# Optimization experiments

Hardware: AMD Instinct MI355X
Metric: run time of the kernel (lower is better)

The kernel has to match this reference:

```python
import jax, jax.numpy as jnp
import numpy as np

B, S, D = 4, 2048, 1024
H = 4 * D          # expert hidden dim
E_SPEC = 4         # num specific experts
E_SHR = 2          # num shared experts
TOP_K = 2


def setup_inputs() -> dict:
    key = jax.random.key(0)
    ks = jax.random.split(key, 16)
    s = 0.02
    return {
        "x": jax.random.normal(ks[0], (B, S, D), jnp.float32),
        # specific experts (stacked over expert axis)
        "spec_w1": jax.random.normal(ks[1], (E_SPEC, D, H), jnp.float32) * s,
        "spec_b1": jnp.zeros((E_SPEC, H), jnp.float32),
        "spec_w2": jax.random.normal(ks[2], (E_SPEC, H, D), jnp.float32) * s,
        "spec_b2": jnp.zeros((E_SPEC, D), jnp.float32),
        "spec_rw": jax.random.normal(ks[3], (D, E_SPEC), jnp.float32) * s,
        "spec_rb": jnp.zeros((E_SPEC,), jnp.float32),
        # shared experts
        "shr_w1": jax.random.normal(ks[4], (E_SHR, D, H), jnp.float32) * s,
        "shr_b1": jnp.zeros((E_SHR, H), jnp.float32),
        "shr_w2": jax.random.normal(ks[5], (E_SHR, H, D), jnp.float32) * s,
        "shr_b2": jnp.zeros((E_SHR, D), jnp.float32),
        "shr_rw": jax.random.normal(ks[6], (D, E_SHR), jnp.float32) * s,
        "shr_rb": jnp.zeros((E_SHR,), jnp.float32),
    }


def _expert_mlp(xf, w1, b1, w2, b2):
    # xf: [T, D]; w1: [E, D, H]; w2: [E, H, D] -> [E, T, D]
    h = jax.nn.gelu(jnp.einsum("td,edh->eth", xf, w1) + b1[:, None, :],
                    approximate=False)
    return jnp.einsum("eth,ehd->etd", h, w2) + b2[:, None, :]


def reference(x, spec_w1, spec_b1, spec_w2, spec_b2, spec_rw, spec_rb,
              shr_w1, shr_b1, shr_w2, shr_b2, shr_rw, shr_rb):
    b, s, d = x.shape
    xf = x.reshape(-1, d)                      # [T, D]
    T = xf.shape[0]

    # --- specific (top-k) routing ---
    spec_probs = jax.nn.softmax(xf @ spec_rw + spec_rb, axis=-1)   # [T, E]
    topk_probs, topk_idx = jax.lax.top_k(spec_probs, TOP_K)        # [T, K]

    # aux load-balancing loss
    counts = jnp.zeros((E_SPEC,), jnp.float32).at[topk_idx.reshape(-1)].add(1.0)
    fraction = counts / (T * TOP_K)
    aux_loss = E_SPEC * jnp.sum(fraction * spec_probs.mean(axis=0))

    # gate[t, e] = sum_k topk_probs[t,k] * 1[topk_idx[t,k]==e]
    gate = jnp.sum(jax.nn.one_hot(topk_idx, E_SPEC, dtype=xf.dtype)
                   * topk_probs[..., None], axis=1)                # [T, E]

    spec_out_e = _expert_mlp(xf, spec_w1, spec_b1, spec_w2, spec_b2)  # [E, T, D]
    specific_out = jnp.einsum("te,etd->td", gate, spec_out_e)

    # --- shared (dense) experts ---
    shr_probs = jax.nn.softmax(xf @ shr_rw + shr_rb, axis=-1)      # [T, E_shr]
    shr_out_e = _expert_mlp(xf, shr_w1, shr_b1, shr_w2, shr_b2)    # [E_shr, T, D]
    shared_out = jnp.einsum("te,etd->td", shr_probs, shr_out_e)

    final = (specific_out + shared_out).reshape(b, s, d)
    return final, aux_loss
```

## Files before the change

kernel.cpp:

```cpp
#include <hip/hip_runtime.h>
#include <hip/hip_bf16.h>

#define T_TOK 8192
#define DDIM 1024
#define HDIM 4096

typedef __bf16 bf16;
typedef bf16 bf16x8 __attribute__((ext_vector_type(8)));
typedef float f32x4 __attribute__((ext_vector_type(4)));

#define ASM_VMCNT(n) asm volatile("s_waitcnt vmcnt(" #n ")" ::: "memory")
#define MFMA16(a, b, c) __builtin_amdgcn_mfma_f32_16x16x32_bf16((a), (b), (c), 0, 0, 0)
#define G8_BAR __builtin_amdgcn_s_barrier()
#define G8_WAIT                                            \
  asm volatile("s_waitcnt lgkmcnt(0)" ::: "memory");       \
  __builtin_amdgcn_sched_barrier(0)

__device__ __forceinline__ void gl_lds16(const void* g, void* l) {
  __builtin_amdgcn_global_load_lds(
      (const __attribute__((address_space(1))) unsigned int*)g,
      (__attribute__((address_space(3))) unsigned int*)l, 16, 0, 0);
}

__device__ __forceinline__ float gelu_f(float v) {
// ... 53 lines not shown
    const float l0 = p0 + srb[0], l1 = p1 + srb[1];
    const float l2 = p2 + srb[2], l3 = p3 + srb[3];
    const float m = fmaxf(fmaxf(l0, l1), fmaxf(l2, l3));
    const float e0 = expf(l0 - m), e1 = expf(l1 - m);
    const float e2 = expf(l2 - m), e3 = expf(l3 - m);
    const float s = e0 + e1 + e2 + e3;
    float pr[4] = {e0 / s, e1 / s, e2 / s, e3 / s};
    int i1 = 0; float v1 = pr[0];
#pragma unroll
    for (int e = 1; e < 4; ++e) if (pr[e] > v1) { v1 = pr[e]; i1 = e; }
    int i2 = -1; float v2 = -1.0f;
#pragma unroll
    for (int e = 0; e < 4; ++e)
      if (e != i1 && pr[e] > v2) { v2 = pr[e]; i2 = e; }
    float g[4] = {0, 0, 0, 0};
    g[i1] = v1; g[i2] = v2;
    float* gr = gate + (size_t)t * 8;
    gr[0] = g[0]; gr[1] = g[1]; gr[2] = g[2]; gr[3] = g[3];
    const float h0 = p4 + hrb[0], h1 = p5 + hrb[1];
    const float mh = fmaxf(h0, h1);
    const float q0 = expf(h0 - mh), q1 = expf(h1 - mh);
    const float qs = q0 + q1;
    gr[4] = q0 / qs; gr[5] = q1 / qs; gr[6] = 0; gr[7] = 0;
    probs4[t] = make_float4(pr[0], pr[1], pr[2], pr[3]);
    top2[t] = i1 | (i2 << 8);
  }
}

__global__ __launch_bounds__(256) void transpose_convert6(
    const float* __restrict__ spec_w, const float* __restrict__ shr_w,
    bf16* __restrict__ dst, int R, int C) {
  __shared__ float tile[32][33];
  const int z = blockIdx.z;
  const float* src = (z < 4) ? spec_w + (size_t)z * R * C
                             : shr_w + (size_t)(z - 4) * R * C;
  bf16* d = dst + (size_t)z * R * C;
  const int c0 = blockIdx.x * 32, r0 = blockIdx.y * 32;
  const int tx = threadIdx.x & 31, ty = threadIdx.x >> 5;
#pragma unroll
  for (int i = 0; i < 4; ++i)
    tile[ty + 8 * i][tx] = src[(size_t)(r0 + ty + 8 * i) * C + c0 + tx];
  __syncthreads();
#pragma unroll
  for (int i = 0; i < 4; ++i)
    d[(size_t)(c0 + ty + 8 * i) * R + r0 + tx] = (bf16)tile[tx][ty + 8 * i];
}

__global__ __launch_bounds__(1024) void scan_build(
    const int* __restrict__ top2, const float4* __restrict__ probs4,
    int* __restrict__ meta, int* __restrict__ lists, int2* __restrict__ tpos,
    float* __restrict__ auxg) {
  __shared__ unsigned long long sc[1024];
  __shared__ float4 rp[512];
  const int tid = threadIdx.x;

  int ee[8];
  unsigned long long c = 0;
  float4 ps = make_float4(0.f, 0.f, 0.f, 0.f);
#pragma unroll
  for (int j = 0; j < 8; ++j) {
    const int t = tid * 8 + j;
    const int p = top2[t];
    ee[j] = p;
    const int a = p & 15, b = (p >> 8) & 15;
    c += (1ULL << (16 * a)) + (1ULL << (16 * b));
    const float4 pv = probs4[t];
    ps.x += pv.x; ps.y += pv.y; ps.z += pv.z; ps.w += pv.w;
  }
  sc[tid] = c;
  __syncthreads();
  for (int off = 1; off < 1024; off <<= 1) {
    const unsigned long long mine = sc[tid];
    const unsigned long long prev = (tid >= off) ? sc[tid - off] : 0ULL;
    __syncthreads();
    sc[tid] = mine + prev;
    __syncthreads();
  }
  const unsigned long long incl = sc[tid];
  const unsigned long long tot = sc[1023];
  const unsigned long long excl = incl - c;
  int q0 = (int)(excl & 0xffff), q1 = (int)((excl >> 16) & 0xffff);
  int q2 = (int)((excl >> 32) & 0xffff), q3 = (int)((excl >> 48) & 0xffff);
#pragma unroll
  for (int j = 0; j < 8; ++j) {
    const int t = tid * 8 + j;
    const int a = ee[j] & 15, b = (ee[j] >> 8) & 15;
    const int pa = (a == 0) ? q0 : (a == 1) ? q1 : (a == 2) ? q2 : q3;
    lists[a * 8192 + pa] = t;
    q0 += (a == 0); q1 += (a == 1); q2 += (a == 2); q3 += (a == 3);
    const int pb = (b == 0) ? q0 : (b == 1) ? q1 : (b == 2) ? q2 : q3;
    lists[b * 8192 + pb] = t;
    q0 += (b == 0); q1 += (b == 1); q2 += (b == 2); q3 += (b == 3);
    tpos[t] = make_int2(a * 8192 + pa, b * 8192 + pb);
  }
  if (tid == 1023) {
    const int c0 = (int)(tot & 0xffff), c1 = (int)((tot >> 16) & 0xffff);
    const int c2 = (int)((tot >> 32) & 0xffff), c3 = (int)((tot >> 48) & 0xffff);
    meta[24] = c0; meta[25] = c1; meta[26] = c2; meta[27] = c3;
    auxg[0] = (float)c0; auxg[1] = (float)c1;
    auxg[2] = (float)c2; auxg[3] = (float)c3;
    const int nb0 = (c0 + 255) >> 8, nb1 = (c1 + 255) >> 8;
    const int nb2 = (c2 + 255) >> 8, nb3 = (c3 + 255) >> 8;
    const int ch0 = (nb0 + 3) >> 2, ch1 = (nb1 + 3) >> 2;
    const int ch2 = (nb2 + 3) >> 2, ch3 = (nb3 + 3) >> 2;
    meta[34] = 0;
    meta[35] = nb0 * 256;
    meta[36] = meta[35] + nb1 * 256;
    meta[37] = meta[36] + nb2 * 256;
    meta[40] = 0;
    meta[41] = 64 * ch0;
    meta[42] = meta[41] + 64 * ch1;
    meta[43] = meta[42] + 64 * ch2;
    meta[44] = meta[43] + 64 * ch3;
    meta[46] = 0;
    meta[47] = 32 * ch0;
    meta[48] = meta[47] + 32 * ch1;
    meta[49] = meta[48] + 32 * ch2;
    meta[50] = meta[49] + 32 * ch3;
  }
  if (tid >= 512) rp[tid - 512] = ps;
  __syncthreads();
  if (tid < 512) {
    const float4 o = rp[tid];
    ps.x += o.x; ps.y += o.y; ps.z += o.z; ps.w += o.w;
  }
  for (int w = 256; w >= 1; w >>= 1) {
    __syncthreads();
    if (tid >= w && tid < 2 * w) rp[tid - w] = ps;
    __syncthreads();
    if (tid < w) {
      const float4 o = rp[tid];
      ps.x += o.x; ps.y += o.y; ps.z += o.z; ps.w += o.w;
    }
  }
  if (tid == 0) {
    auxg[4] = ps.x; auxg[5] = ps.y; auxg[6] = ps.z; auxg[7] = ps.w;
  }
}

__global__ void aux_finalize(const float* __restrict__ auxg,
                             float* __restrict__ outp) {
  float a = 0.0f;
#pragma unroll
  for (int e = 0; e < 4; ++e)
    a += (auxg[e] / (float)(T_TOK * 2)) * (auxg[4 + e] / (float)T_TOK);
  outp[0] = 4.0f * a;
}

template <int KIND>
__global__ __launch_bounds__(512, 2) void g8(
    const bf16* __restrict__ A, const bf16* __restrict__ Bw,
    const float* __restrict__ bias, bf16* __restrict__ h_all, int N,
    int CH_M, int CH_N, const int* __restrict__ meta,
    const int* __restrict__ lists, const float* __restrict__ gate) {
  __shared__ __align__(1024) bf16 Alds[2 * 256 * 64];
  __shared__ __align__(1024) bf16 Blds[2 * 256 * 64];

  const int tid = threadIdx.x;
  const int lane = tid & 63, wid = tid >> 6;
  const int wm = wid >> 2, wn = wid & 3;
  const int lr = lane & 15, lg = lane >> 4;

  int bm, bn, hb = 0, s = 0;
  const bf16* Bp = Bw;
  const float* biasp = bias;
  if constexpr (KIND == 0) {
    const int xcd = blockIdx.x & 7, idx = blockIdx.x >> 3;
    bm = (xcd >> 1) * CH_M + idx / CH_N;
    bn = (xcd & 1) * CH_N + idx % CH_N;
  } else {
    const int b = blockIdx.x;
    if (b >= meta[44]) return;
    s = (b >= meta[41]) + (b >= meta[42]) + (b >= meta[43]);
    const int local = b - meta[40 + s];
    const int nbm = (meta[24 + s] + 255) >> 8;
    const int CHm = (nbm + 3) >> 2;
    if (local >= 64 * CHm) return;
    const int xc = local & 7, idx = local >> 3;
    bm = (xc >> 1) * CHm + idx / 8;
    bn = (xc & 1) * 8 + idx % 8;
    if (bm >= nbm) return;
    hb = meta[34 + s];
    Bp = Bw + (size_t)s * DDIM * HDIM;
    biasp = bias + (size_t)s * HDIM;
  }
  const int K = DDIM;
  const int NT = K >> 6;

  const int rl = tid >> 3;
  const int cbs = ((tid * 16) & 127) ^ ((rl & 7) << 4);
  int ar[4];
#pragma unroll
  for (int c = 0; c < 4; ++c) ar[c] = bm * 256 + c * 64 + rl;
  if constexpr (KIND != 0) {
    const int* lp = lists + s * 8192;
#pragma unroll
    for (int c = 0; c < 4; ++c) {
      const int t = lp[ar[c]];
      ar[c] = t < 0 ? 0 : t;
    }
  }
  const bf16* sA[4];
  const bf16* sB[4];
#pragma unroll
  for (int c = 0; c < 4; ++c) {
    sA[c] = A + (size_t)ar[c] * K + (cbs >> 1);
    sB[c] = Bp + (size_t)(bn * 256 + c * 64 + rl) * K + (cbs >> 1);
  }
  char* const ldsA = (char*)Alds;
  char* const ldsB = (char*)Blds;
  const int wb = wid * 1024;

  const int ax0 = (lg * 16) ^ ((lr & 7) << 4);
  const int ax1 = ax0 ^ 64;
  const int aro = (wm * 128 + lr) * 128;
  const int bro = (wn * 64 + lr) * 128;
  const char* const A0 = (const char*)Alds + aro + ax0;
  const char* const A1 = (const char*)Alds + aro + ax1;
  const char* const B0 = (const char*)Blds + bro + ax0;
  const char* const B1 = (const char*)Blds + bro + ax1;

  f32x4 acc[8][4] = {};
  bf16x8 af[4][2], b01[2][2], b23[2][2];

#define G8_RA(BOFF, MB)                                               \
  _Pragma("unroll") for (int i = 0; i < 4; ++i) {                     \
    af[i][0] = *(const bf16x8*)(A0 + (BOFF) + ((MB) + i) * 2048);     \
    af[i][1] = *(const bf16x8*)(A1 + (BOFF) + ((MB) + i) * 2048);     \
  }
#define G8_RB(BOFF, DST, NB)                                          \
  _Pragma("unroll") for (int i = 0; i < 2; ++i) {                     \
    DST[i][0] = *(const bf16x8*)(B0 + (BOFF) + ((NB) + i) * 2048);    \
    DST[i][1] = *(const bf16x8*)(B1 + (BOFF) + ((NB) + i) * 2048);    \
  }
#define G8_MMA(MB, NB, BSRC)                                          \
  __builtin_amdgcn_s_setprio(1);                                      \
  _Pragma("unroll") for (int i = 0; i < 4; ++i)                       \
    _Pragma("unroll") for (int j = 0; j < 2; ++j) {                   \
      acc[(MB) + i][(NB) + j] =                                       \
          MFMA16(af[i][0], BSRC[j][0], acc[(MB) + i][(NB) + j]);      \
      acc[(MB) + i][(NB) + j] =                                       \
          MFMA16(af[i][1], BSRC[j][1], acc[(MB) + i][(NB) + j]);      \
    }                                                                 \
  __builtin_amdgcn_s_setprio(0);
#define G8_STG_B(T, C, BUFO)                                          \
  gl_lds16(sB[C] + (size_t)(T) * 64, ldsB + (BUFO) + (C) * 8192 + wb);
#define G8_STG_A(T, C, BUFO)                                          \
  gl_lds16(sA[C] + (size_t)(T) * 64, ldsA + (BUFO) + (C) * 8192 + wb);

  G8_STG_B(0, 0, 0) G8_STG_B(0, 1, 0) G8_STG_B(0, 2, 0) G8_STG_B(0, 3, 0)
  G8_STG_A(0, 0, 0) G8_STG_A(0, 1, 0) G8_STG_A(0, 2, 0) G8_STG_A(0, 3, 0)
  G8_STG_B(1, 0, 32768) G8_STG_B(1, 1, 32768)
  G8_STG_B(1, 2, 32768) G8_STG_B(1, 3, 32768)
  G8_STG_A(1, 0, 32768) G8_STG_A(1, 1, 32768)
  G8_STG_A(1, 2, 32768) G8_STG_A(1, 3, 32768)
  ASM_VMCNT(8);
  G8_BAR;

  for (int t = 0; t < NT; t += 2) {
    const bool stg = (t + 2) < NT;
    G8_RA(0, 0);
    G8_RB(0, b01, 0);
    G8_BAR; G8_WAIT;
    G8_MMA(0, 0, b01);
    G8_BAR;
    G8_RB(0, b23, 2);
    G8_BAR; G8_WAIT;
    G8_MMA(0, 2, b23);
    G8_BAR;
    G8_RA(0, 4);
    if (stg) { G8_STG_B(t + 2, 0, 0) G8_STG_B(t + 2, 1, 0) }
    G8_BAR; G8_WAIT;
    G8_MMA(4, 0, b01);
    G8_BAR;
    if (stg) { G8_STG_B(t + 2, 2, 0) G8_STG_B(t + 2, 3, 0) }
    G8_MMA(4, 2, b23);
    if (stg) ASM_VMCNT(4); else ASM_VMCNT(0);
    G8_BAR;
    G8_RA(32768, 0);
    G8_RB(32768, b01, 0);
    if (stg) { G8_STG_A(t + 2, 0, 0) G8_STG_A(t + 2, 1, 0) }
    G8_BAR; G8_WAIT;
    G8_MMA(0, 0, b01);
    G8_BAR;
    G8_RB(32768, b23, 2);
    if (stg) { G8_STG_A(t + 2, 2, 0) G8_STG_A(t + 2, 3, 0) }
    G8_BAR; G8_WAIT;
    G8_MMA(0, 2, b23);
    G8_BAR;
    G8_RA(32768, 4);
    if (stg) {
      G8_STG_B(t + 3, 0, 32768) G8_STG_B(t + 3, 1, 32768)
      G8_STG_B(t + 3, 2, 32768) G8_STG_B(t + 3, 3, 32768)
    }
    G8_BAR; G8_WAIT;
    G8_MMA(4, 0, b01);
    G8_BAR;
    if (stg) {
      G8_STG_A(t + 3, 0, 32768) G8_STG_A(t + 3, 1, 32768)
      G8_STG_A(t + 3, 2, 32768) G8_STG_A(t + 3, 3, 32768)
    }
    G8_MMA(4, 2, b23);
    if (stg) ASM_VMCNT(8);
    G8_BAR;
  }

  const int colb = bn * 256 + wn * 64;
  const int rowb = bm * 256 + wm * 128 + lg * 4;
  float bv[4];
#pragma unroll
  for (int nf = 0; nf < 4; ++nf) bv[nf] = biasp[colb + nf * 16 + lr];
  const int sgid = (KIND == 0) ? 4 + (bn >> 4) : s;
#pragma unroll
  for (int mf = 0; mf < 8; ++mf) {
    float gv[4];
#pragma unroll
    for (int r = 0; r < 4; ++r) {
      const int lrow = rowb + mf * 16 + r;
      if constexpr (KIND == 0) {
        gv[r] = gate[(size_t)lrow * 8 + sgid];
      } else {
        const int tok = lists[s * 8192 + lrow];
        gv[r] = tok >= 0 ? gate[(size_t)tok * 8 + sgid] : 0.0f;
      }
    }
#pragma unroll
    for (int nf = 0; nf < 4; ++nf) {
      const int col = colb + nf * 16 + lr;
#pragma unroll
      for (int r = 0; r < 4; ++r) {
        const int row = hb + rowb + mf * 16 + r;
        h_all[(size_t)row * N + col] =
            (bf16)(gv[r] * gelu_f(acc[mf][nf][r] + bv[nf]));
      }
    }
  }
}

__global__ __launch_bounds__(512, 2) void g2sh(
    const bf16* __restrict__ A, const bf16* __restrict__ w2_0,
    const bf16* __restrict__ w2_1, const float* __restrict__ b2,
    float* __restrict__ out, const float* __restrict__ gate) {
  __shared__ __align__(1024) bf16 Alds[2 * 256 * 64];
  __shared__ __align__(1024) bf16 Blds[2 * 128 * 64];

  const int tid = threadIdx.x;
  const int lane = tid & 63, wid = tid >> 6;
  const int wm = wid >> 2, wn = wid & 3;
  const int lr = lane & 15, lg = lane >> 4;

  const int xcd = blockIdx.x & 7, idx = blockIdx.x >> 3;
  const int bm = (xcd >> 1) * 8 + idx / 4;
  const int bn = (xcd & 1) * 4 + idx % 4;
  const int lda = 8192, N = DDIM;
  const int NT = 128;

  const int L = tid * 16;
  const int rl = L >> 7;
  const int colb = (L & 127) ^ ((rl & 7) << 4);

  const int ar0 = bm * 256 + rl;
  const bf16* sAc0 = A + (size_t)ar0 * lda + (colb >> 1);
  const bf16* sAc1 = A + (size_t)(ar0 + 64) * lda + (colb >> 1);
  const bf16* sAc2 = A + (size_t)(ar0 + 128) * lda + (colb >> 1);
  const bf16* sAc3 = A + (size_t)(ar0 + 192) * lda + (colb >> 1);
  const bf16* pB[2][2];
  pB[0][0] = w2_0 + (size_t)(bn * 128 + rl) * 4096 + (colb >> 1);
  pB[0][1] = w2_0 + (size_t)(bn * 128 + 64 + rl) * 4096 + (colb >> 1);
  pB[1][0] = w2_1 + (size_t)(bn * 128 + rl) * 4096 + (colb >> 1);
  pB[1][1] = w2_1 + (size_t)(bn * 128 + 64 + rl) * 4096 + (colb >> 1);

  char* const ldsA = (char*)Alds;
  char* const ldsB = (char*)Blds;
  const int wb = wid * 1024;
  char* const stA[2] = {ldsA + wb, ldsA + 32768 + wb};
  char* const stB[2] = {ldsB + wb, ldsB + 16384 + wb};

  const int ax0 = (lg * 16) ^ ((lr & 7) << 4);
  const int ax1 = ax0 ^ 64;
  const int aro = (wm * 128 + lr) * 128;
  const int bro = (wn * 32 + lr) * 128;
  const char* const Ak0[2] = {ldsA + aro + ax0, ldsA + 32768 + aro + ax0};
  const char* const Ak1[2] = {ldsA + aro + ax1, ldsA + 32768 + aro + ax1};
  const char* const Bk0[2] = {ldsB + bro + ax0, ldsB + 16384 + bro + ax0};
  const char* const Bk1[2] = {ldsB + bro + ax1, ldsB + 16384 + bro + ax1};

  f32x4 acc[8][2] = {};

#define G2S_STB(T, DST)                                                   \
  {                                                                       \
    const int hh = (T) >> 6;                                              \
    const size_t oo = (size_t)((T) & 63) * 64;                            \
    gl_lds16(pB[hh][0] + oo, DST);                                        \
    gl_lds16(pB[hh][1] + oo, DST + 8192);                                 \
  }

  gl_lds16(sAc0, stA[0]);
  gl_lds16(sAc1, stA[0] + 8192);
  gl_lds16(sAc2, stA[0] + 16384);
  gl_lds16(sAc3, stA[0] + 24576);
  G2S_STB(0, stB[0])
  G2S_STB(1, stB[1])
  gl_lds16(sAc0 + 64, stA[1]);
  gl_lds16(sAc1 + 64, stA[1] + 8192);
  ASM_VMCNT(4);
  __builtin_amdgcn_s_barrier();

  for (int kt0 = 0; kt0 < NT; kt0 += 2) {
#pragma unroll
    for (int par = 0; par < 2; ++par) {
      const int kt = kt0 + par;
      const int cur = par, oth = par ^ 1;
      const bool st1 = (kt + 1) < NT, st2 = (kt + 2) < NT;
      const size_t ko1 = (size_t)(kt + 1) << 6, ko2 = (size_t)(kt + 2) << 6;
      const char* Ac0 = Ak0[cur]; const char* Ac1 = Ak1[cur];
      const char* Bc0 = Bk0[cur]; const char* Bc1 = Bk1[cur];

      bf16x8 af[4][2], bfr[2][2];

#pragma unroll
      for (int mf = 0; mf < 4; ++mf) {
        af[mf][0] = *(const bf16x8*)(Ac0 + mf * 2048);
        af[mf][1] = *(const bf16x8*)(Ac1 + mf * 2048);
      }
      bfr[0][0] = *(const bf16x8*)(Bc0);
      bfr[0][1] = *(const bf16x8*)(Bc1);
      if (st1) {
        gl_lds16(sAc2 + ko1, stA[oth] + 16384);
        gl_lds16(sAc3 + ko1, stA[oth] + 24576);
      }
      __builtin_amdgcn_s_barrier();
      asm volatile("s_waitcnt lgkmcnt(0)" ::: "memory");
      __builtin_amdgcn_sched_barrier(0);
      __builtin_amdgcn_s_setprio(1);
#pragma unroll
      for (int mf = 0; mf < 4; ++mf) {
        acc[mf][0] = MFMA16(af[mf][0], bfr[0][0], acc[mf][0]);
        acc[mf][0] = MFMA16(af[mf][1], bfr[0][1], acc[mf][0]);
      }
      __builtin_amdgcn_s_setprio(0);
      __builtin_amdgcn_s_barrier();

      bfr[1][0] = *(const bf16x8*)(Bc0 + 2048);
      bfr[1][1] = *(const bf16x8*)(Bc1 + 2048);
      __builtin_amdgcn_s_barrier();
      asm volatile("s_waitcnt lgkmcnt(0)" ::: "memory");
      __builtin_amdgcn_sched_barrier(0);
      __builtin_amdgcn_s_setprio(1);
#pragma unroll
      for (int mf = 0; mf < 4; ++mf) {
        acc[mf][1] = MFMA16(af[mf][0], bfr[1][0], acc[mf][1]);
        acc[mf][1] = MFMA16(af[mf][1], bfr[1][1], acc[mf][1]);
      }
      __builtin_amdgcn_s_setprio(0);
      __builtin_amdgcn_s_barrier();

#pragma unroll
      for (int mf = 0; mf < 4; ++mf) {
        af[mf][0] = *(const bf16x8*)(Ac0 + 8192 + mf * 2048);
        af[mf][1] = *(const bf16x8*)(Ac1 + 8192 + mf * 2048);
      }
      if (st2) G2S_STB(kt + 2, stB[cur])
      __builtin_amdgcn_s_barrier();
      asm volatile("s_waitcnt lgkmcnt(0)" ::: "memory");
      __builtin_amdgcn_sched_barrier(0);
      __builtin_amdgcn_s_setprio(1);
#pragma unroll
      for (int mf = 0; mf < 4; ++mf) {
        acc[4 + mf][0] = MFMA16(af[mf][0], bfr[0][0], acc[4 + mf][0]);
        acc[4 + mf][0] = MFMA16(af[mf][1], bfr[0][1], acc[4 + mf][0]);
      }
      __builtin_amdgcn_s_setprio(0);
      __builtin_amdgcn_s_barrier();

      if (st2) {
        gl_lds16(sAc0 + ko2, stA[cur]);
        gl_lds16(sAc1 + ko2, stA[cur] + 8192);
      }
      __builtin_amdgcn_s_setprio(1);
#pragma unroll
      for (int mf = 0; mf < 4; ++mf) {
        acc[4 + mf][1] = MFMA16(af[mf][0], bfr[1][0], acc[4 + mf][1]);
        acc[4 + mf][1] = MFMA16(af[mf][1], bfr[1][1], acc[4 + mf][1]);
      }
      __builtin_amdgcn_s_setprio(0);
      if (st2) {
        ASM_VMCNT(4);
        __builtin_amdgcn_s_barrier();
      } else if (st1) {
        ASM_VMCNT(0);
        __builtin_amdgcn_s_barrier();
      }
    }
  }

  const int colb2 = bn * 128 + wn * 32;
  const int rowb = bm * 256 + wm * 128 + lg * 4;
  float bv0[2], bv1[2];
#pragma unroll
  for (int nf = 0; nf < 2; ++nf) {
    bv0[nf] = b2[colb2 + nf * 16 + lr];
    bv1[nf] = b2[1024 + colb2 + nf * 16 + lr];
  }
#pragma unroll
  for (int mf = 0; mf < 8; ++mf) {
    float g4[4], g5[4];
#pragma unroll
    for (int r = 0; r < 4; ++r) {
      const size_t row = rowb + mf * 16 + r;
      g4[r] = gate[row * 8 + 4];
      g5[r] = gate[row * 8 + 5];
    }
#pragma unroll
    for (int nf = 0; nf < 2; ++nf) {
      const int col = colb2 + nf * 16 + lr;
#pragma unroll
      for (int r = 0; r < 4; ++r) {
        out[(size_t)(rowb + mf * 16 + r) * N + col] =
            acc[mf][nf][r] + g4[r] * bv0[nf] + g5[r] * bv1[nf];
      }
    }
  }
}

template <int PMODE>
__global__ __launch_bounds__(512, 2) void g2sp(
    const bf16* __restrict__ h_all, const bf16* __restrict__ w2t,
    const float* __restrict__ spec_b2, float* __restrict__ out,
    bf16* __restrict__ P, const float* __restrict__ gate,
    const int* __restrict__ meta, const int* __restrict__ lists, int e) {
  __shared__ __align__(1024) bf16 Alds[2 * 256 * 64];
  __shared__ __align__(1024) bf16 Blds[2 * 128 * 64];

  const int tid = threadIdx.x;
  const int lane = tid & 63, wid = tid >> 6;
  const int wm = wid >> 2, wn = wid & 3;
  const int lr = lane & 15, lg = lane >> 4;

  int bm, bn, s = e;
  if constexpr (PMODE == 1) {
    const int b = blockIdx.x;
    if (b >= meta[50]) return;
    s = (b >= meta[47]) + (b >= meta[48]) + (b >= meta[49]);
    const int local = b - meta[46 + s];
    const int nbm = (meta[24 + s] + 255) >> 8;
    const int CHm = (nbm + 3) >> 2;
    if (local >= 32 * CHm) return;
    const int xc = local & 7, idx = local >> 3;
    bm = (xc >> 1) * CHm + idx / 4;
    bn = (xc & 1) * 4 + idx % 4;
    if (bm >= nbm) return;
  } else {
    const int nbm = (meta[24 + e] + 255) >> 8;
    const int CHm = (nbm + 3) >> 2;
    if (blockIdx.x >= 8 * CHm * 4) return;
    const int xc = blockIdx.x & 7, idx = blockIdx.x >> 3;
    bm = (xc >> 1) * CHm + idx / 4;
    bn = (xc & 1) * 4 + idx % 4;
    if (bm >= nbm) return;
  }
  const int hb = meta[34 + s];
  const bf16* B = w2t + (size_t)s * DDIM * HDIM;
  const float* bias = spec_b2 + (size_t)s * DDIM;
  const int K = HDIM, N = DDIM;
  const int NT = K >> 6;

  const int L = tid * 16;
  const int rl = L >> 7;
  const int colb = (L & 127) ^ ((rl & 7) << 4);

  const int ar0 = hb + bm * 256 + rl;
  const bf16* sAc0 = h_all + (size_t)ar0 * K + (colb >> 1);
  const bf16* sAc1 = h_all + (size_t)(ar0 + 64) * K + (colb >> 1);
  const bf16* sAc2 = h_all + (size_t)(ar0 + 128) * K + (colb >> 1);
  const bf16* sAc3 = h_all + (size_t)(ar0 + 192) * K + (colb >> 1);
  const bf16* sB = B + (size_t)(bn * 128 + rl) * K + (colb >> 1);

  char* const ldsA = (char*)Alds;
  char* const ldsB = (char*)Blds;
  const int wb = wid * 1024;
  char* const stA[2] = {ldsA + wb, ldsA + 32768 + wb};
  char* const stB[2] = {ldsB + wb, ldsB + 16384 + wb};

  const int ax0 = (lg * 16) ^ ((lr & 7) << 4);
  const int ax1 = ax0 ^ 64;
  const int aro = (wm * 128 + lr) * 128;
  const int bro = (wn * 32 + lr) * 128;
  const char* const Ak0[2] = {ldsA + aro + ax0, ldsA + 32768 + aro + ax0};
  const char* const Ak1[2] = {ldsA + aro + ax1, ldsA + 32768 + aro + ax1};
  const char* const Bk0[2] = {ldsB + bro + ax0, ldsB + 16384 + bro + ax0};
  const char* const Bk1[2] = {ldsB + bro + ax1, ldsB + 16384 + bro + ax1};

  f32x4 acc[8][2] = {};

  gl_lds16(sAc0, stA[0]);
  gl_lds16(sAc1, stA[0] + 8192);
  gl_lds16(sAc2, stA[0] + 16384);
  gl_lds16(sAc3, stA[0] + 24576);
  gl_lds16(sB, stB[0]);
  gl_lds16(sB + (size_t)64 * K, stB[0] + 8192);
  gl_lds16(sB + 64, stB[1]);
  gl_lds16(sB + (size_t)64 * K + 64, stB[1] + 8192);
  gl_lds16(sAc0 + 64, stA[1]);
  gl_lds16(sAc1 + 64, stA[1] + 8192);
  ASM_VMCNT(4);
  __builtin_amdgcn_s_barrier();

  for (int kt0 = 0; kt0 < NT; kt0 += 2) {
#pragma unroll
    for (int par = 0; par < 2; ++par) {
      const int kt = kt0 + par;
      const int cur = par, oth = par ^ 1;
      const bool st1 = (kt + 1) < NT, st2 = (kt + 2) < NT;
      const size_t ko1 = (size_t)(kt + 1) << 6, ko2 = (size_t)(kt + 2) << 6;
      const char* Ac0 = Ak0[cur]; const char* Ac1 = Ak1[cur];
      const char* Bc0 = Bk0[cur]; const char* Bc1 = Bk1[cur];

      bf16x8 af[4][2], bfr[2][2];

#pragma unroll
      for (int mf = 0; mf < 4; ++mf) {
        af[mf][0] = *(const bf16x8*)(Ac0 + mf * 2048);
        af[mf][1] = *(const bf16x8*)(Ac1 + mf * 2048);
      }
      bfr[0][0] = *(const bf16x8*)(Bc0);
      bfr[0][1] = *(const bf16x8*)(Bc1);
      if (st1) {
        gl_lds16(sAc2 + ko1, stA[oth] + 16384);
        gl_lds16(sAc3 + ko1, stA[oth] + 24576);
      }
      __builtin_amdgcn_s_barrier();
      asm volatile("s_waitcnt lgkmcnt(0)" ::: "memory");
      __builtin_amdgcn_sched_barrier(0);
      __builtin_amdgcn_s_setprio(1);
#pragma unroll
      for (int mf = 0; mf < 4; ++mf) {
        acc[mf][0] = MFMA16(af[mf][0], bfr[0][0], acc[mf][0]);
        acc[mf][0] = MFMA16(af[mf][1], bfr[0][1], acc[mf][0]);
      }
      __builtin_amdgcn_s_setprio(0);
      __builtin_amdgcn_s_barrier();

      bfr[1][0] = *(const bf16x8*)(Bc0 + 2048);
      bfr[1][1] = *(const bf16x8*)(Bc1 + 2048);
      __builtin_amdgcn_s_barrier();
      asm volatile("s_waitcnt lgkmcnt(0)" ::: "memory");
      __builtin_amdgcn_sched_barrier(0);
      __builtin_amdgcn_s_setprio(1);
#pragma unroll
      for (int mf = 0; mf < 4; ++mf) {
        acc[mf][1] = MFMA16(af[mf][0], bfr[1][0], acc[mf][1]);
        acc[mf][1] = MFMA16(af[mf][1], bfr[1][1], acc[mf][1]);
      }
      __builtin_amdgcn_s_setprio(0);
      __builtin_amdgcn_s_barrier();

#pragma unroll
      for (int mf = 0; mf < 4; ++mf) {
        af[mf][0] = *(const bf16x8*)(Ac0 + 8192 + mf * 2048);
        af[mf][1] = *(const bf16x8*)(Ac1 + 8192 + mf * 2048);
      }
      if (st2) {
        gl_lds16(sB + ko2, stB[cur]);
        gl_lds16(sB + (size_t)64 * K + ko2, stB[cur] + 8192);
      }
      __builtin_amdgcn_s_barrier();
      asm volatile("s_waitcnt lgkmcnt(0)" ::: "memory");
      __builtin_amdgcn_sched_barrier(0);
      __builtin_amdgcn_s_setprio(1);
#pragma unroll
      for (int mf = 0; mf < 4; ++mf) {
        acc[4 + mf][0] = MFMA16(af[mf][0], bfr[0][0], acc[4 + mf][0]);
        acc[4 + mf][0] = MFMA16(af[mf][1], bfr[0][1], acc[4 + mf][0]);
      }
      __builtin_amdgcn_s_setprio(0);
      __builtin_amdgcn_s_barrier();

      if (st2) {
        gl_lds16(sAc0 + ko2, stA[cur]);
        gl_lds16(sAc1 + ko2, stA[cur] + 8192);
      }
      __builtin_amdgcn_s_setprio(1);
#pragma unroll
      for (int mf = 0; mf < 4; ++mf) {
        acc[4 + mf][1] = MFMA16(af[mf][0], bfr[1][0], acc[4 + mf][1]);
        acc[4 + mf][1] = MFMA16(af[mf][1], bfr[1][1], acc[4 + mf][1]);
      }
      __builtin_amdgcn_s_setprio(0);
      if (st2) {
        ASM_VMCNT(4);
        __builtin_amdgcn_s_barrier();
      } else if (st1) {
        ASM_VMCNT(0);
        __builtin_amdgcn_s_barrier();
      }
    }
  }

  const int colb2 = bn * 128 + wn * 32;
  const int rowb = bm * 256 + wm * 128 + lg * 4;
  float bv[2];
#pragma unroll
  for (int nf = 0; nf < 2; ++nf) bv[nf] = bias[colb2 + nf * 16 + lr];
  const int* lp = lists + s * 8192;
#pragma unroll
  for (int mf = 0; mf < 8; ++mf) {
    int tok[4]; float gv[4];
#pragma unroll
    for (int r = 0; r < 4; ++r) {
      tok[r] = lp[rowb + mf * 16 + r];
      gv[r] = tok[r] >= 0 ? gate[(size_t)tok[r] * 8 + s] : 0.0f;
    }
#pragma unroll
    for (int nf = 0; nf < 2; ++nf) {
      const int col = colb2 + nf * 16 + lr;
#pragma unroll
      for (int r = 0; r < 4; ++r) {
        const float v = acc[mf][nf][r] + gv[r] * bv[nf];
        if constexpr (PMODE == 1) {
          P[(size_t)(hb + rowb + mf * 16 + r) * N + col] = (bf16)v;
        } else {
          if (tok[r] >= 0) out[(size_t)tok[r] * N + col] += v;
        }
      }
    }
  }
}

__global__ __launch_bounds__(256) void reduce_spec(
    const bf16* __restrict__ P, const int2* __restrict__ tpos,
    const int* __restrict__ meta, float* __restrict__ out) {
  const int t = blockIdx.x;
  const int c = threadIdx.x * 4;
  const int2 tp = tpos[t];
  const int ea = tp.x >> 13, pa = tp.x & 8191;
  const int eb = tp.y >> 13, pb = tp.y & 8191;
  const size_t ra = (size_t)(meta[34 + ea] + pa) * DDIM + c;
  const size_t rb = (size_t)(meta[34 + eb] + pb) * DDIM + c;
  const bf16x8* pav = (const bf16x8*)&P[ra];
  float4 o = *(float4*)&out[(size_t)t * DDIM + c];
  const bf16* A4 = &P[ra];
  const bf16* B4 = &P[rb];
  o.x += (float)A4[0] + (float)B4[0];
  o.y += (float)A4[1] + (float)B4[1];
  o.z += (float)A4[2] + (float)B4[2];
  o.w += (float)A4[3] + (float)B4[3];
  (void)pav;
  *(float4*)&out[(size_t)t * DDIM + c] = o;
}

extern "C" void kernel_launch(void* const* d_in, const int* in_sizes, int n_in,
                              void* d_out, int out_size, void* d_ws,
                              size_t ws_size, hipStream_t stream) {
  const float* x = (const float*)d_in[0];
  const float* spec_w1 = (const float*)d_in[1];
  const float* spec_b1 = (const float*)d_in[2];
  const float* spec_w2 = (const float*)d_in[3];
  const float* spec_b2 = (const float*)d_in[4];
  const float* spec_rw = (const float*)d_in[5];
  const float* spec_rb = (const float*)d_in[6];
  const float* shr_w1 = (const float*)d_in[7];
  const float* shr_b1 = (const float*)d_in[8];
  const float* shr_w2 = (const float*)d_in[9];
  const float* shr_b2 = (const float*)d_in[10];
  const float* shr_rw = (const float*)d_in[11];
  const float* shr_rb = (const float*)d_in[12];
  float* out = (float*)d_out;

  char* ws = (char*)d_ws;
  const size_t DH = (size_t)DDIM * HDIM;
  const size_t OFF_W1 = 16777216;
  const size_t OFF_W2 = OFF_W1 + 50331648;
  const size_t OFF_GATE = OFF_W2 + 50331648;
  const size_t OFF_AUX = OFF_GATE + 262144;
  const size_t OFF_META = OFF_AUX + 256;
  const size_t OFF_LIST = OFF_META + 256;
  const size_t OFF_T2 = OFF_LIST + 131072;
  const size_t OFF_P4 = OFF_T2 + 32768;
  const size_t OFF_TPOS = OFF_P4 + 131072 + 1024;
  const size_t OFF_H = OFF_TPOS + 65536;
  const size_t H_BYTES = (size_t)17408 * HDIM * 2;
  const size_t OFF_P = OFF_H + H_BYTES;
  const size_t P_BYTES = (size_t)17408 * DDIM * 2;
  bf16* xb = (bf16*)ws;
  bf16* w1t = (bf16*)(ws + OFF_W1);
  bf16* w2t = (bf16*)(ws + OFF_W2);
  float* gate = (float*)(ws + OFF_GATE);
  float* auxg = (float*)(ws + OFF_AUX);
  int* meta = (int*)(ws + OFF_META);
  int* lists = (int*)(ws + OFF_LIST);
  int* top2 = (int*)(ws + OFF_T2);
  float4* probs4 = (float4*)(ws + OFF_P4);
  int2* tpos = (int2*)(ws + OFF_TPOS);
  bf16* h = (bf16*)(ws + OFF_H);
  bf16* P = (bf16*)(ws + OFF_P);

  const bool ppath = ws_size >= OFF_P + P_BYTES;

  hipMemsetAsync(lists, 0xFF, 4 * 8192 * 4, stream);

  conv_router<<<T_TOK / 4, 256, 0, stream>>>(x, xb, spec_rw, spec_rb, shr_rw,
                                             shr_rb, gate, probs4, top2);
  scan_build<<<1, 1024, 0, stream>>>(top2, probs4, meta, lists, tpos, auxg);

  transpose_convert6<<<dim3(HDIM / 32, DDIM / 32, 6), 256, 0, stream>>>(
      spec_w1, shr_w1, w1t, DDIM, HDIM);
  transpose_convert6<<<dim3(DDIM / 32, HDIM / 32, 6), 256, 0, stream>>>(
      spec_w2, shr_w2, w2t, HDIM, DDIM);

  g8<0><<<1024, 512, 0, stream>>>(xb, w1t + 4 * DH, shr_b1, h, 8192,
                                  8, 16, meta, lists, gate);
  g2sh<<<256, 512, 0, stream>>>(h, w2t + 4 * DH, w2t + 5 * DH, shr_b2, out,
                                gate);
  g8<1><<<2048, 512, 0, stream>>>(xb, w1t, spec_b1, h, 4096,
                                  0, 8, meta, lists, gate);
  if (ppath) {
    g2sp<1><<<1024, 512, 0, stream>>>(h, w2t, spec_b2, out, P, gate, meta,
                                      lists, 0);
    reduce_spec<<<T_TOK, 256, 0, stream>>>(P, tpos, meta, out);
  } else {
    for (int e = 0; e < 4; ++e)
      g2sp<0><<<256, 512, 0, stream>>>(h, w2t, spec_b2, out, nullptr, gate,
                                       meta, lists, e);
  }
  aux_finalize<<<1, 1, 0, stream>>>(auxg, out + (size_t)T_TOK * DDIM);
}
```

Baseline: 1.062 ms.

## Move gate scaling to second GEMM epilogue and split shared expert down-projection

The gate multiply moves out of the first GEMM's GELU epilogue, so h stores plain GELU activations, and is applied in the second GEMM epilogue as gate*(acc+bias). The fused two-expert shared down-projection kernel is replaced by a generic g2k kernel launched twice, the second accumulating into out with a read-modify-write. The partial-sum buffer P now reuses the w1t workspace region, so the P path always runs and the per-expert fallback is removed. This trims the first GEMM epilogue and drops the workspace-size dependence, at the cost of an extra launch and an extra read and write of out for the shared experts.

```diff
diff --git a/kernel.cpp b/kernel.cpp
--- a/kernel.cpp
+++ b/kernel.cpp
@@ -229,7 +229,7 @@
     const bf16* __restrict__ A, const bf16* __restrict__ Bw,
     const float* __restrict__ bias, bf16* __restrict__ h_all, int N,
     int CH_M, int CH_N, const int* __restrict__ meta,
-    const int* __restrict__ lists, const float* __restrict__ gate) {
+    const int* __restrict__ lists) {
   __shared__ __align__(1024) bf16 Alds[2 * 256 * 64];
   __shared__ __align__(1024) bf16 Blds[2 * 256 * 64];
 
@@ -383,41 +383,28 @@
   }
 
   const int colb = bn * 256 + wn * 64;
-  const int rowb = bm * 256 + wm * 128 + lg * 4;
+  const int rowb = hb + bm * 256 + wm * 128 + lg * 4;
   float bv[4];
 #pragma unroll
   for (int nf = 0; nf < 4; ++nf) bv[nf] = biasp[colb + nf * 16 + lr];
-  const int sgid = (KIND == 0) ? 4 + (bn >> 4) : s;
-#pragma unroll
-  for (int mf = 0; mf < 8; ++mf) {
-    float gv[4];
-#pragma unroll
-    for (int r = 0; r < 4; ++r) {
-      const int lrow = rowb + mf * 16 + r;
-      if constexpr (KIND == 0) {
-        gv[r] = gate[(size_t)lrow * 8 + sgid];
-      } else {
-        const int tok = lists[s * 8192 + lrow];
-        gv[r] = tok >= 0 ? gate[(size_t)tok * 8 + sgid] : 0.0f;
-      }
-    }
+#pragma unroll
+  for (int mf = 0; mf < 8; ++mf)
 #pragma unroll
     for (int nf = 0; nf < 4; ++nf) {
       const int col = colb + nf * 16 + lr;
 #pragma unroll
       for (int r = 0; r < 4; ++r) {
-        const int row = hb + rowb + mf * 16 + r;
-        h_all[(size_t)row * N + col] =
-            (bf16)(gv[r] * gelu_f(acc[mf][nf][r] + bv[nf]));
-      }
-    }
-  }
-}
-
-__global__ __launch_bounds__(512, 2) void g2sh(
-    const bf16* __restrict__ A, const bf16* __restrict__ w2_0,
-    const bf16* __restrict__ w2_1, const float* __restrict__ b2,
-    float* __restrict__ out, const float* __restrict__ gate) {
+        const int row = rowb + mf * 16 + r;
+        h_all[(size_t)row * N + col] = (bf16)gelu_f(acc[mf][nf][r] + bv[nf]);
+      }
+    }
+}
+
+template <int EMODE>
+__global__ __launch_bounds__(512, 2) void g2k(
+    const bf16* __restrict__ A, int lda, const bf16* __restrict__ B,
+    const float* __restrict__ bias, float* __restrict__ out,
+    const float* __restrict__ gate, int gidx) {
   __shared__ __align__(1024) bf16 Alds[2 * 256 * 64];
   __shared__ __align__(1024) bf16 Blds[2 * 128 * 64];
 
@@ -429,8 +416,8 @@
   const int xcd = blockIdx.x & 7, idx = blockIdx.x >> 3;
   const int bm = (xcd >> 1) * 8 + idx / 4;
   const int bn = (xcd & 1) * 4 + idx % 4;
-  const int lda = 8192, N = DDIM;
-  const int NT = 128;
+  const int K = HDIM, N = DDIM;
+  const int NT = K >> 6;
 
   const int L = tid * 16;
   const int rl = L >> 7;
@@ -441,216 +428,6 @@
   const bf16* sAc1 = A + (size_t)(ar0 + 64) * lda + (colb >> 1);
   const bf16* sAc2 = A + (size_t)(ar0 + 128) * lda + (colb >> 1);
   const bf16* sAc3 = A + (size_t)(ar0 + 192) * lda + (colb >> 1);
-  const bf16* pB[2][2];
-  pB[0][0] = w2_0 + (size_t)(bn * 128 + rl) * 4096 + (colb >> 1);
-  pB[0][1] = w2_0 + (size_t)(bn * 128 + 64 + rl) * 4096 + (colb >> 1);
-  pB[1][0] = w2_1 + (size_t)(bn * 128 + rl) * 4096 + (colb >> 1);
-  pB[1][1] = w2_1 + (size_t)(bn * 128 + 64 + rl) * 4096 + (colb >> 1);
-
-  char* const ldsA = (char*)Alds;
-  char* const ldsB = (char*)Blds;
-  const int wb = wid * 1024;
-  char* const stA[2] = {ldsA + wb, ldsA + 32768 + wb};
-  char* const stB[2] = {ldsB + wb, ldsB + 16384 + wb};
-
-  const int ax0 = (lg * 16) ^ ((lr & 7) << 4);
-  const int ax1 = ax0 ^ 64;
-  const int aro = (wm * 128 + lr) * 128;
-  const int bro = (wn * 32 + lr) * 128;
-  const char* const Ak0[2] = {ldsA + aro + ax0, ldsA + 32768 + aro + ax0};
-  const char* const Ak1[2] = {ldsA + aro + ax1, ldsA + 32768 + aro + ax1};
-  const char* const Bk0[2] = {ldsB + bro + ax0, ldsB + 16384 + bro + ax0};
-  const char* const Bk1[2] = {ldsB + bro + ax1, ldsB + 16384 + bro + ax1};
-
-  f32x4 acc[8][2] = {};
-
-#define G2S_STB(T, DST)                                                   \
-  {                                                                       \
-    const int hh = (T) >> 6;                                              \
-    const size_t oo = (size_t)((T) & 63) * 64;                            \
-    gl_lds16(pB[hh][0] + oo, DST);                                        \
-    gl_lds16(pB[hh][1] + oo, DST + 8192);                                 \
-  }
-
-  gl_lds16(sAc0, stA[0]);
-  gl_lds16(sAc1, stA[0] + 8192);
-  gl_lds16(sAc2, stA[0] + 16384);
-  gl_lds16(sAc3, stA[0] + 24576);
-  G2S_STB(0, stB[0])
-  G2S_STB(1, stB[1])
-  gl_lds16(sAc0 + 64, stA[1]);
-  gl_lds16(sAc1 + 64, stA[1] + 8192);
-  ASM_VMCNT(4);
-  __builtin_amdgcn_s_barrier();
-
-  for (int kt0 = 0; kt0 < NT; kt0 += 2) {
-#pragma unroll
-    for (int par = 0; par < 2; ++par) {
-      const int kt = kt0 + par;
-      const int cur = par, oth = par ^ 1;
-      const bool st1 = (kt + 1) < NT, st2 = (kt + 2) < NT;
-      const size_t ko1 = (size_t)(kt + 1) << 6, ko2 = (size_t)(kt + 2) << 6;
-      const char* Ac0 = Ak0[cur]; const char* Ac1 = Ak1[cur];
-      const char* Bc0 = Bk0[cur]; const char* Bc1 = Bk1[cur];
-
-      bf16x8 af[4][2], bfr[2][2];
-
-#pragma unroll
-      for (int mf = 0; mf < 4; ++mf) {
-        af[mf][0] = *(const bf16x8*)(Ac0 + mf * 2048);
-        af[mf][1] = *(const bf16x8*)(Ac1 + mf * 2048);
-      }
-      bfr[0][0] = *(const bf16x8*)(Bc0);
-      bfr[0][1] = *(const bf16x8*)(Bc1);
-      if (st1) {
-        gl_lds16(sAc2 + ko1, stA[oth] + 16384);
-        gl_lds16(sAc3 + ko1, stA[oth] + 24576);
-      }
-      __builtin_amdgcn_s_barrier();
-      asm volatile("s_waitcnt lgkmcnt(0)" ::: "memory");
-      __builtin_amdgcn_sched_barrier(0);
-      __builtin_amdgcn_s_setprio(1);
-#pragma unroll
-      for (int mf = 0; mf < 4; ++mf) {
-        acc[mf][0] = MFMA16(af[mf][0], bfr[0][0], acc[mf][0]);
-        acc[mf][0] = MFMA16(af[mf][1], bfr[0][1], acc[mf][0]);
-      }
-      __builtin_amdgcn_s_setprio(0);
-      __builtin_amdgcn_s_barrier();
-
-      bfr[1][0] = *(const bf16x8*)(Bc0 + 2048);
-      bfr[1][1] = *(const bf16x8*)(Bc1 + 2048);
-      __builtin_amdgcn_s_barrier();
-      asm volatile("s_waitcnt lgkmcnt(0)" ::: "memory");
-      __builtin_amdgcn_sched_barrier(0);
-      __builtin_amdgcn_s_setprio(1);
-#pragma unroll
-      for (int mf = 0; mf < 4; ++mf) {
-        acc[mf][1] = MFMA16(af[mf][0], bfr[1][0], acc[mf][1]);
-        acc[mf][1] = MFMA16(af[mf][1], bfr[1][1], acc[mf][1]);
-      }
-      __builtin_amdgcn_s_setprio(0);
-      __builtin_amdgcn_s_barrier();
-
-#pragma unroll
-      for (int mf = 0; mf < 4; ++mf) {
-        af[mf][0] = *(const bf16x8*)(Ac0 + 8192 + mf * 2048);
-        af[mf][1] = *(const bf16x8*)(Ac1 + 8192 + mf * 2048);
-      }
-      if (st2) G2S_STB(kt + 2, stB[cur])
-      __builtin_amdgcn_s_barrier();
-      asm volatile("s_waitcnt lgkmcnt(0)" ::: "memory");
-      __builtin_amdgcn_sched_barrier(0);
-      __builtin_amdgcn_s_setprio(1);
-#pragma unroll
-      for (int mf = 0; mf < 4; ++mf) {
-        acc[4 + mf][0] = MFMA16(af[mf][0], bfr[0][0], acc[4 + mf][0]);
-        acc[4 + mf][0] = MFMA16(af[mf][1], bfr[0][1], acc[4 + mf][0]);
-      }
-      __builtin_amdgcn_s_setprio(0);
-      __builtin_amdgcn_s_barrier();
-
-      if (st2) {
-        gl_lds16(sAc0 + ko2, stA[cur]);
-        gl_lds16(sAc1 + ko2, stA[cur] + 8192);
-      }
-      __builtin_amdgcn_s_setprio(1);
-#pragma unroll
-      for (int mf = 0; mf < 4; ++mf) {
-        acc[4 + mf][1] = MFMA16(af[mf][0], bfr[1][0], acc[4 + mf][1]);
-        acc[4 + mf][1] = MFMA16(af[mf][1], bfr[1][1], acc[4 + mf][1]);
-      }
-      __builtin_amdgcn_s_setprio(0);
-      if (st2) {
-        ASM_VMCNT(4);
-        __builtin_amdgcn_s_barrier();
-      } else if (st1) {
-        ASM_VMCNT(0);
-        __builtin_amdgcn_s_barrier();
-      }
-    }
-  }
-
-  const int colb2 = bn * 128 + wn * 32;
-  const int rowb = bm * 256 + wm * 128 + lg * 4;
-  float bv0[2], bv1[2];
-#pragma unroll
-  for (int nf = 0; nf < 2; ++nf) {
-    bv0[nf] = b2[colb2 + nf * 16 + lr];
-    bv1[nf] = b2[1024 + colb2 + nf * 16 + lr];
-  }
-#pragma unroll
-  for (int mf = 0; mf < 8; ++mf) {
-    float g4[4], g5[4];
-#pragma unroll
-    for (int r = 0; r < 4; ++r) {
-      const size_t row = rowb + mf * 16 + r;
-      g4[r] = gate[row * 8 + 4];
-      g5[r] = gate[row * 8 + 5];
-    }
-#pragma unroll
-    for (int nf = 0; nf < 2; ++nf) {
-      const int col = colb2 + nf * 16 + lr;
-#pragma unroll
-      for (int r = 0; r < 4; ++r) {
-        out[(size_t)(rowb + mf * 16 + r) * N + col] =
-            acc[mf][nf][r] + g4[r] * bv0[nf] + g5[r] * bv1[nf];
-      }
-    }
-  }
-}
-
-template <int PMODE>
-__global__ __launch_bounds__(512, 2) void g2sp(
-    const bf16* __restrict__ h_all, const bf16* __restrict__ w2t,
-    const float* __restrict__ spec_b2, float* __restrict__ out,
-    bf16* __restrict__ P, const float* __restrict__ gate,
-    const int* __restrict__ meta, const int* __restrict__ lists, int e) {
-  __shared__ __align__(1024) bf16 Alds[2 * 256 * 64];
-  __shared__ __align__(1024) bf16 Blds[2 * 128 * 64];
-
-  const int tid = threadIdx.x;
-  const int lane = tid & 63, wid = tid >> 6;
-  const int wm = wid >> 2, wn = wid & 3;
-  const int lr = lane & 15, lg = lane >> 4;
-
-  int bm, bn, s = e;
-  if constexpr (PMODE == 1) {
-    const int b = blockIdx.x;
-    if (b >= meta[50]) return;
-    s = (b >= meta[47]) + (b >= meta[48]) + (b >= meta[49]);
-    const int local = b - meta[46 + s];
-    const int nbm = (meta[24 + s] + 255) >> 8;
-    const int CHm = (nbm + 3) >> 2;
-    if (local >= 32 * CHm) return;
-    const int xc = local & 7, idx = local >> 3;
-    bm = (xc >> 1) * CHm + idx / 4;
-    bn = (xc & 1) * 4 + idx % 4;
-    if (bm >= nbm) return;
-  } else {
-    const int nbm = (meta[24 + e] + 255) >> 8;
-    const int CHm = (nbm + 3) >> 2;
-    if (blockIdx.x >= 8 * CHm * 4) return;
-    const int xc = blockIdx.x & 7, idx = blockIdx.x >> 3;
-    bm = (xc >> 1) * CHm + idx / 4;
-    bn = (xc & 1) * 4 + idx % 4;
-    if (bm >= nbm) return;
-  }
-  const int hb = meta[34 + s];
-  const bf16* B = w2t + (size_t)s * DDIM * HDIM;
-  const float* bias = spec_b2 + (size_t)s * DDIM;
-  const int K = HDIM, N = DDIM;
-  const int NT = K >> 6;
-
-  const int L = tid * 16;
-  const int rl = L >> 7;
-  const int colb = (L & 127) ^ ((rl & 7) << 4);
-
-  const int ar0 = hb + bm * 256 + rl;
-  const bf16* sAc0 = h_all + (size_t)ar0 * K + (colb >> 1);
-  const bf16* sAc1 = h_all + (size_t)(ar0 + 64) * K + (colb >> 1);
-  const bf16* sAc2 = h_all + (size_t)(ar0 + 128) * K + (colb >> 1);
-  const bf16* sAc3 = h_all + (size_t)(ar0 + 192) * K + (colb >> 1);
   const bf16* sB = B + (size_t)(bn * 128 + rl) * K + (colb >> 1);
 
   char* const ldsA = (char*)Alds;
@@ -779,6 +556,196 @@
   float bv[2];
 #pragma unroll
   for (int nf = 0; nf < 2; ++nf) bv[nf] = bias[colb2 + nf * 16 + lr];
+#pragma unroll
+  for (int mf = 0; mf < 8; ++mf) {
+    float gv[4];
+#pragma unroll
+    for (int r = 0; r < 4; ++r)
+      gv[r] = gate[(size_t)(rowb + mf * 16 + r) * 8 + gidx];
+#pragma unroll
+    for (int nf = 0; nf < 2; ++nf) {
+      const int col = colb2 + nf * 16 + lr;
+#pragma unroll
+      for (int r = 0; r < 4; ++r) {
+        const float v = acc[mf][nf][r] + bv[nf];
+        const size_t oi = (size_t)(rowb + mf * 16 + r) * N + col;
+        if constexpr (EMODE == 1)
+          out[oi] += gv[r] * v;
+        else
+          out[oi] = gv[r] * v;
+      }
+    }
+  }
+}
+
+__global__ __launch_bounds__(512, 2) void g2sp(
+    const bf16* __restrict__ h_all, const bf16* __restrict__ w2t,
+    const float* __restrict__ spec_b2, bf16* __restrict__ P,
+    const float* __restrict__ gate, const int* __restrict__ meta,
+    const int* __restrict__ lists) {
+  __shared__ __align__(1024) bf16 Alds[2 * 256 * 64];
+  __shared__ __align__(1024) bf16 Blds[2 * 128 * 64];
+
+  const int tid = threadIdx.x;
+  const int lane = tid & 63, wid = tid >> 6;
+  const int wm = wid >> 2, wn = wid & 3;
+  const int lr = lane & 15, lg = lane >> 4;
+
+  const int b = blockIdx.x;
+  if (b >= meta[50]) return;
+  const int s = (b >= meta[47]) + (b >= meta[48]) + (b >= meta[49]);
+  const int local = b - meta[46 + s];
+  const int nbm = (meta[24 + s] + 255) >> 8;
+  const int CHm = (nbm + 3) >> 2;
+  if (local >= 32 * CHm) return;
+  const int xc = local & 7, idx = local >> 3;
+  int bm = (xc >> 1) * CHm + idx / 4;
+  int bn = (xc & 1) * 4 + idx % 4;
+  if (bm >= nbm) return;
+
+  const int hb = meta[34 + s];
+  const bf16* B = w2t + (size_t)s * DDIM * HDIM;
+  const float* bias = spec_b2 + (size_t)s * DDIM;
+  const int K = HDIM, N = DDIM;
+  const int NT = K >> 6;
+
+  const int L = tid * 16;
+  const int rl = L >> 7;
+  const int colb = (L & 127) ^ ((rl & 7) << 4);
+
+  const int ar0 = hb + bm * 256 + rl;
+  const bf16* sAc0 = h_all + (size_t)ar0 * K + (colb >> 1);
+  const bf16* sAc1 = h_all + (size_t)(ar0 + 64) * K + (colb >> 1);
+  const bf16* sAc2 = h_all + (size_t)(ar0 + 128) * K + (colb >> 1);
+  const bf16* sAc3 = h_all + (size_t)(ar0 + 192) * K + (colb >> 1);
+  const bf16* sB = B + (size_t)(bn * 128 + rl) * K + (colb >> 1);
+
+  char* const ldsA = (char*)Alds;
+  char* const ldsB = (char*)Blds;
+  const int wb = wid * 1024;
+  char* const stA[2] = {ldsA + wb, ldsA + 32768 + wb};
+  char* const stB[2] = {ldsB + wb, ldsB + 16384 + wb};
+
+  const int ax0 = (lg * 16) ^ ((lr & 7) << 4);
+  const int ax1 = ax0 ^ 64;
+  const int aro = (wm * 128 + lr) * 128;
+  const int bro = (wn * 32 + lr) * 128;
+  const char* const Ak0[2] = {ldsA + aro + ax0, ldsA + 32768 + aro + ax0};
+  const char* const Ak1[2] = {ldsA + aro + ax1, ldsA + 32768 + aro + ax1};
+  const char* const Bk0[2] = {ldsB + bro + ax0, ldsB + 16384 + bro + ax0};
+  const char* const Bk1[2] = {ldsB + bro + ax1, ldsB + 16384 + bro + ax1};
+
+  f32x4 acc[8][2] = {};
+
+  gl_lds16(sAc0, stA[0]);
+  gl_lds16(sAc1, stA[0] + 8192);
+  gl_lds16(sAc2, stA[0] + 16384);
+  gl_lds16(sAc3, stA[0] + 24576);
+  gl_lds16(sB, stB[0]);
+  gl_lds16(sB + (size_t)64 * K, stB[0] + 8192);
+  gl_lds16(sB + 64, stB[1]);
+  gl_lds16(sB + (size_t)64 * K + 64, stB[1] + 8192);
+  gl_lds16(sAc0 + 64, stA[1]);
+  gl_lds16(sAc1 + 64, stA[1] + 8192);
+  ASM_VMCNT(4);
+  __builtin_amdgcn_s_barrier();
+
+  for (int kt0 = 0; kt0 < NT; kt0 += 2) {
+#pragma unroll
+    for (int par = 0; par < 2; ++par) {
+      const int kt = kt0 + par;
+      const int cur = par, oth = par ^ 1;
+      const bool st1 = (kt + 1) < NT, st2 = (kt + 2) < NT;
+      const size_t ko1 = (size_t)(kt + 1) << 6, ko2 = (size_t)(kt + 2) << 6;
+      const char* Ac0 = Ak0[cur]; const char* Ac1 = Ak1[cur];
+      const char* Bc0 = Bk0[cur]; const char* Bc1 = Bk1[cur];
+
+      bf16x8 af[4][2], bfr[2][2];
+
+#pragma unroll
+      for (int mf = 0; mf < 4; ++mf) {
+        af[mf][0] = *(const bf16x8*)(Ac0 + mf * 2048);
+        af[mf][1] = *(const bf16x8*)(Ac1 + mf * 2048);
+      }
+      bfr[0][0] = *(const bf16x8*)(Bc0);
+      bfr[0][1] = *(const bf16x8*)(Bc1);
+      if (st1) {
+        gl_lds16(sAc2 + ko1, stA[oth] + 16384);
+        gl_lds16(sAc3 + ko1, stA[oth] + 24576);
+      }
+      __builtin_amdgcn_s_barrier();
+      asm volatile("s_waitcnt lgkmcnt(0)" ::: "memory");
+      __builtin_amdgcn_sched_barrier(0);
+      __builtin_amdgcn_s_setprio(1);
+#pragma unroll
+      for (int mf = 0; mf < 4; ++mf) {
+        acc[mf][0] = MFMA16(af[mf][0], bfr[0][0], acc[mf][0]);
+        acc[mf][0] = MFMA16(af[mf][1], bfr[0][1], acc[mf][0]);
+      }
+      __builtin_amdgcn_s_setprio(0);
+      __builtin_amdgcn_s_barrier();
+
+      bfr[1][0] = *(const bf16x8*)(Bc0 + 2048);
+      bfr[1][1] = *(const bf16x8*)(Bc1 + 2048);
+      __builtin_amdgcn_s_barrier();
+      asm volatile("s_waitcnt lgkmcnt(0)" ::: "memory");
+      __builtin_amdgcn_sched_barrier(0);
+      __builtin_amdgcn_s_setprio(1);
+#pragma unroll
+      for (int mf = 0; mf < 4; ++mf) {
+        acc[mf][1] = MFMA16(af[mf][0], bfr[1][0], acc[mf][1]);
+        acc[mf][1] = MFMA16(af[mf][1], bfr[1][1], acc[mf][1]);
+      }
+      __builtin_amdgcn_s_setprio(0);
+      __builtin_amdgcn_s_barrier();
+
+#pragma unroll
+      for (int mf = 0; mf < 4; ++mf) {
+        af[mf][0] = *(const bf16x8*)(Ac0 + 8192 + mf * 2048);
+        af[mf][1] = *(const bf16x8*)(Ac1 + 8192 + mf * 2048);
+      }
+      if (st2) {
+        gl_lds16(sB + ko2, stB[cur]);
+        gl_lds16(sB + (size_t)64 * K + ko2, stB[cur] + 8192);
+      }
+      __builtin_amdgcn_s_barrier();
+      asm volatile("s_waitcnt lgkmcnt(0)" ::: "memory");
+      __builtin_amdgcn_sched_barrier(0);
+      __builtin_amdgcn_s_setprio(1);
+#pragma unroll
+      for (int mf = 0; mf < 4; ++mf) {
+        acc[4 + mf][0] = MFMA16(af[mf][0], bfr[0][0], acc[4 + mf][0]);
+        acc[4 + mf][0] = MFMA16(af[mf][1], bfr[0][1], acc[4 + mf][0]);
+      }
+      __builtin_amdgcn_s_setprio(0);
+      __builtin_amdgcn_s_barrier();
+
+      if (st2) {
+        gl_lds16(sAc0 + ko2, stA[cur]);
+        gl_lds16(sAc1 + ko2, stA[cur] + 8192);
+      }
+      __builtin_amdgcn_s_setprio(1);
+#pragma unroll
+      for (int mf = 0; mf < 4; ++mf) {
+        acc[4 + mf][1] = MFMA16(af[mf][0], bfr[1][0], acc[4 + mf][1]);
+        acc[4 + mf][1] = MFMA16(af[mf][1], bfr[1][1], acc[4 + mf][1]);
+      }
+      __builtin_amdgcn_s_setprio(0);
+      if (st2) {
+        ASM_VMCNT(4);
+        __builtin_amdgcn_s_barrier();
+      } else if (st1) {
+        ASM_VMCNT(0);
+        __builtin_amdgcn_s_barrier();
+      }
+    }
+  }
+
+  const int colb2 = bn * 128 + wn * 32;
+  const int rowb = bm * 256 + wm * 128 + lg * 4;
+  float bv[2];
+#pragma unroll
+  for (int nf = 0; nf < 2; ++nf) bv[nf] = bias[colb2 + nf * 16 + lr];
   const int* lp = lists + s * 8192;
 #pragma unroll
   for (int mf = 0; mf < 8; ++mf) {
@@ -793,12 +760,8 @@
       const int col = colb2 + nf * 16 + lr;
 #pragma unroll
       for (int r = 0; r < 4; ++r) {
-        const float v = acc[mf][nf][r] + gv[r] * bv[nf];
-        if constexpr (PMODE == 1) {
-          P[(size_t)(hb + rowb + mf * 16 + r) * N + col] = (bf16)v;
-        } else {
-          if (tok[r] >= 0) out[(size_t)tok[r] * N + col] += v;
-        }
+        const float v = gv[r] * (acc[mf][nf][r] + bv[nf]);
+        P[(size_t)(hb + rowb + mf * 16 + r) * N + col] = (bf16)v;
       }
     }
   }
@@ -812,17 +775,13 @@
   const int2 tp = tpos[t];
   const int ea = tp.x >> 13, pa = tp.x & 8191;
   const int eb = tp.y >> 13, pb = tp.y & 8191;
-  const size_t ra = (size_t)(meta[34 + ea] + pa) * DDIM + c;
-  const size_t rb = (size_t)(meta[34 + eb] + pb) * DDIM + c;
-  const bf16x8* pav = (const bf16x8*)&P[ra];
+  const bf16* A4 = &P[(size_t)(meta[34 + ea] + pa) * DDIM + c];
+  const bf16* B4 = &P[(size_t)(meta[34 + eb] + pb) * DDIM + c];
   float4 o = *(float4*)&out[(size_t)t * DDIM + c];
-  const bf16* A4 = &P[ra];
-  const bf16* B4 = &P[rb];
   o.x += (float)A4[0] + (float)B4[0];
   o.y += (float)A4[1] + (float)B4[1];
   o.z += (float)A4[2] + (float)B4[2];
   o.w += (float)A4[3] + (float)B4[3];
-  (void)pav;
   *(float4*)&out[(size_t)t * DDIM + c] = o;
 }
 
@@ -856,9 +815,6 @@
   const size_t OFF_P4 = OFF_T2 + 32768;
   const size_t OFF_TPOS = OFF_P4 + 131072 + 1024;
   const size_t OFF_H = OFF_TPOS + 65536;
-  const size_t H_BYTES = (size_t)17408 * HDIM * 2;
-  const size_t OFF_P = OFF_H + H_BYTES;
-  const size_t P_BYTES = (size_t)17408 * DDIM * 2;
   bf16* xb = (bf16*)ws;
   bf16* w1t = (bf16*)(ws + OFF_W1);
   bf16* w2t = (bf16*)(ws + OFF_W2);
@@ -870,9 +826,7 @@
   float4* probs4 = (float4*)(ws + OFF_P4);
   int2* tpos = (int2*)(ws + OFF_TPOS);
   bf16* h = (bf16*)(ws + OFF_H);
-  bf16* P = (bf16*)(ws + OFF_P);
-
-  const bool ppath = ws_size >= OFF_P + P_BYTES;
+  bf16* P = w1t;
 
   hipMemsetAsync(lists, 0xFF, 4 * 8192 * 4, stream);
 
@@ -886,19 +840,15 @@
       spec_w2, shr_w2, w2t, HDIM, DDIM);
 
   g8<0><<<1024, 512, 0, stream>>>(xb, w1t + 4 * DH, shr_b1, h, 8192,
-                                  8, 16, meta, lists, gate);
-  g2sh<<<256, 512, 0, stream>>>(h, w2t + 4 * DH, w2t + 5 * DH, shr_b2, out,
-                                gate);
+                                  8, 16, meta, lists);
+  g2k<0><<<256, 512, 0, stream>>>(h, 8192, w2t + 4 * DH, shr_b2, out,
+                                  gate, 4);
+  g2k<1><<<256, 512, 0, stream>>>(h + 4096, 8192, w2t + 5 * DH,
+                                  shr_b2 + 1024, out, gate, 5);
   g8<1><<<2048, 512, 0, stream>>>(xb, w1t, spec_b1, h, 4096,
-                                  0, 8, meta, lists, gate);
-  if (ppath) {
-    g2sp<1><<<1024, 512, 0, stream>>>(h, w2t, spec_b2, out, P, gate, meta,
-                                      lists, 0);
-    reduce_spec<<<T_TOK, 256, 0, stream>>>(P, tpos, meta, out);
-  } else {
-    for (int e = 0; e < 4; ++e)
-      g2sp<0><<<256, 512, 0, stream>>>(h, w2t, spec_b2, out, nullptr, gate,
-                                       meta, lists, e);
-  }
+                                  0, 8, meta, lists);
+  g2sp<<<1024, 512, 0, stream>>>(h, w2t, spec_b2, P, gate, meta, lists);
+  reduce_spec<<<T_TOK, 256, 0, stream>>>(P, tpos, meta, out);
+
   aux_finalize<<<1, 1, 0, stream>>>(auxg, out + (size_t)T_TOK * DDIM);
 }
```

New measurement: 888.7 us (median of 2 runs). 16.3% less time.
